# Performance work log

Hardware: AMD Instinct MI355X
Metric: run time of the kernel (lower is better)

## Reference

```python
import jax, jax.numpy as jnp
import numpy as np

N = 2000        # num_genes (nodes)
E = 64000       # edges
Q = 200000      # query edges
F_IN = 512      # num_features
H = 64          # hidden
Q_PHASE = 0.25  # magnetic charge q
SIM_DIM = 64
LABELS = 2


def _msconv(xr, xi, src, dst, w, W, n):
    """MagNet/MSGNN Chebyshev conv, K=1, sym normalization, absolute degree.

    A_s = (A + A^T)/2, Theta_ij = 2*pi*q*(A_ij - A_ji),
    L_hat = L - I = -D^{-1/2} A_s D^{-1/2} * exp(i*Theta)  (lambda_max = 2)
    out = X @ W[0] + (L_hat X) @ W[1]   (real weights on complex signal)
    """
    # symmetrize: each directed edge contributes entries (src->dst) and (dst->src)
    ss = jnp.concatenate([src, dst])
    dd = jnp.concatenate([dst, src])
    ws = jnp.concatenate([w, w]) * 0.5
    theta = 2.0 * jnp.pi * Q_PHASE * jnp.concatenate([w, -w])
    # absolute degree of symmetrized adjacency
    deg = jax.ops.segment_sum(jnp.abs(ws), dd, num_segments=n)
    dinv = jnp.where(deg > 0, 1.0 / jnp.sqrt(deg), 0.0)
    norm = ws * dinv[ss] * dinv[dd]
    cr = -norm * jnp.cos(theta)  # real part of L_hat entries
    ci = -norm * jnp.sin(theta)  # imag part
    xrs, xis = xr[ss], xi[ss]
    t1r = jax.ops.segment_sum(cr[:, None] * xrs - ci[:, None] * xis, dd, num_segments=n)
    t1i = jax.ops.segment_sum(cr[:, None] * xis + ci[:, None] * xrs, dd, num_segments=n)
    return xr @ W[0] + t1r @ W[1], xi @ W[0] + t1i @ W[1]


def setup_inputs() -> dict:
    key = jax.random.key(0)
    ks = jax.random.split(key, 10)
    real = jax.random.normal(ks[0], (N, F_IN), jnp.float32)
    imag = jax.random.normal(ks[1], (N, F_IN), jnp.float32)
    edge_index = jax.random.randint(ks[2], (2, E), 0, N, dtype=jnp.int64)
    query_edges = jax.random.randint(ks[3], (Q, 2), 0, N, dtype=jnp.int64)
    all_embeddings = jax.random.normal(ks[4], (N * N, SIM_DIM), jnp.float32)
    edge_weight = jax.random.uniform(ks[5], (E,), jnp.float32)
    W1 = jax.random.normal(ks[6], (2, F_IN, H), jnp.float32) / np.sqrt(F_IN)
    W2 = jax.random.normal(ks[7], (2, H, H), jnp.float32) / np.sqrt(H)
    lin_w = jax.random.normal(ks[8], (4 * H + SIM_DIM, LABELS), jnp.float32) * 0.05
    lin_b = jnp.zeros((LABELS,), jnp.float32)
    return {"real": real, "imag": imag, "edge_index": edge_index,
            "query_edges": query_edges, "all_embeddings": all_embeddings,
            "edge_weight": edge_weight, "W1": W1, "W2": W2,
            "lin_w": lin_w, "lin_b": lin_b}


def reference(real, imag, edge_index, query_edges, all_embeddings, edge_weight,
              W1, W2, lin_w, lin_b):
    src, dst = edge_index[0], edge_index[1]
    for W in (W1, W2):
        real, imag = _msconv(real, imag, src, dst, edge_weight, W, N)
        mask = (real >= 0).astype(real.dtype)   # complex_relu
        real = real * mask
        imag = imag * mask
    ni, nj = query_edges[:, 0], query_edges[:, 1]
    sim = all_embeddings[ni * N + nj]           # vectorized per-edge lookup
    x = jnp.concatenate([real[ni], real[nj], imag[ni], imag[nj], sim], axis=-1)
    # eval mode: dropout is identity
    logits = x @ lin_w + lin_b
    return jax.nn.log_softmax(logits, axis=1)
```

## Files before the change

kernel.cpp:

```cpp
#include <hip/hip_runtime.h>
#include <math.h>

constexpr int N_NODES = 2000;
constexpr int F_IN    = 512;
constexpr int H       = 64;
constexpr int SLOT_SH = 8;
constexpr int GBLK    = 1664;

__device__ __forceinline__ void gemm_tile256(
    const float* __restrict__ A, const float* __restrict__ W,
    float (*As)[33], float (*Ws)[64],
    int r0, int K, float* __restrict__ C)
{
  int t  = threadIdx.x;
  int tx = t & 15, ty = t >> 4;
  float acc[4][4] = {};
  for (int k0 = 0; k0 < K; k0 += 32) {
    #pragma unroll
    for (int i = 0; i < 8; i++) {
      int idx = t + i * 256;
      int row = idx >> 5, kk = idx & 31;
      int gr = r0 + row;
      As[row][kk] = (gr < N_NODES) ? A[(size_t)gr * K + k0 + kk] : 0.f;
    }
    #pragma unroll
    for (int i = 0; i < 8; i++) {
      int idx = t + i * 256;
      int kk = idx >> 6, col = idx & 63;
      Ws[kk][col] = W[(size_t)(k0 + kk) * H + col];
    }
    __syncthreads();
    #pragma unroll
    for (int kk = 0; kk < 32; kk++) {
      float4 wv = *reinterpret_cast<const float4*>(&Ws[kk][tx * 4]);
      float av[4];
      #pragma unroll
      for (int r = 0; r < 4; r++) av[r] = As[ty * 4 + r][kk];
      #pragma unroll
      for (int r = 0; r < 4; r++) {
        acc[r][0] = fmaf(av[r], wv.x, acc[r][0]);
        acc[r][1] = fmaf(av[r], wv.y, acc[r][1]);
        acc[r][2] = fmaf(av[r], wv.z, acc[r][2]);
        acc[r][3] = fmaf(av[r], wv.w, acc[r][3]);
      }
    }
    __syncthreads();
  }
  #pragma unroll
  for (int r = 0; r < 4; r++) {
    int gr = r0 + ty * 4 + r;
    if (gr < N_NODES) {
      *reinterpret_cast<float4*>(&C[(size_t)gr * H + tx * 4]) =
          make_float4(acc[r][0], acc[r][1], acc[r][2], acc[r][3]);
    }
  }
}

__global__ __launch_bounds__(256) void mega_kernel(
    const float* __restrict__ real, const float* __restrict__ imag,
    const float* __restrict__ W1,
    const int* __restrict__ ei, const float* __restrict__ ew,
    const int* __restrict__ qe, const float* __restrict__ emb,
    const float* __restrict__ lw,
    float* __restrict__ deg, int* __restrict__ cnt,
    int* __restrict__ nbr, float* __restrict__ cra, float* __restrict__ cia,
    float* __restrict__ P0r, float* __restrict__ P0i,
    float* __restrict__ P1r, float* __restrict__ P1i,
    float2* __restrict__ sl, int E, int Qn, int eblocks)
{
  __shared__ float As[64][33];
  __shared__ float Ws[32][64];
  int b = blockIdx.x;
  if (b < GBLK) {
    const float2* lw2 = reinterpret_cast<const float2*>(lw);
    int l = threadIdx.x & 15;
    float2 wa = lw2[256 + 4 * l];
    float2 wb = lw2[257 + 4 * l];
    float2 wc = lw2[258 + 4 * l];
    float2 wd = lw2[259 + 4 * l];
    int g0 = (b * 256 + threadIdx.x) >> 4;
    int ng = (GBLK * 256) >> 4;
    const float4* emb4 = reinterpret_cast<const float4*>(emb);
    for (int q = g0; q < Qn; q += 2 * ng) {
      int q2 = q + ng;
      bool has2 = q2 < Qn;
      int ni0 = qe[2 * q], nj0 = qe[2 * q + 1];
      int ni1 = has2 ? qe[2 * q2] : ni0;
      int nj1 = has2 ? qe[2 * q2 + 1] : nj0;
      float4 sa = emb4[((size_t)ni0 * N_NODES + nj0) * 16 + l];
      float4 sb = emb4[((size_t)ni1 * N_NODES + nj1) * 16 + l];
      float a0 = sa.x * wa.x + sa.y * wb.x + sa.z * wc.x + sa.w * wd.x;
      float a1 = sa.x * wa.y + sa.y * wb.y + sa.z * wc.y + sa.w * wd.y;
      float b0 = sb.x * wa.x + sb.y * wb.x + sb.z * wc.x + sb.w * wd.x;
      float b1 = sb.x * wa.y + sb.y * wb.y + sb.z * wc.y + sb.w * wd.y;
      #pragma unroll
      for (int off = 1; off < 16; off <<= 1) {
        a0 += __shfl_xor(a0, off, 64);
        a1 += __shfl_xor(a1, off, 64);
        b0 += __shfl_xor(b0, off, 64);
        b1 += __shfl_xor(b1, off, 64);
      }
      if (l == 0) {
        sl[q] = make_float2(a0, a1);
        if (has2) sl[q2] = make_float2(b0, b1);
      }
    }
  } else if (b < GBLK + eblocks) {
    int e = (b - GBLK) * 256 + threadIdx.x;
    if (e < E) {
      int s = ei[e], d = ei[E + e];
      float ww = ew[e];
      float aw = fabsf(0.5f * ww);
      atomicAdd(&deg[d], aw);
      atomicAdd(&deg[s], aw);
      float sn, cs;
      sincosf(1.5707963267948966f * ww, &sn, &cs);
      float cr = -0.5f * ww * cs;
      float ci = -0.5f * ww * sn;
      int p1 = atomicAdd(&cnt[d], 1);
      int i1 = (d << SLOT_SH) + p1;
      nbr[i1] = s; cra[i1] = cr; cia[i1] = ci;
      int p2 = atomicAdd(&cnt[s], 1);
      int i2 = (s << SLOT_SH) + p2;
      nbr[i2] = d; cra[i2] = cr; cia[i2] = -ci;
    }
  } else {
    int bi = b - GBLK - eblocks;
    int which = bi & 3, tile = bi >> 2;
    const float* A = (which & 1) ? imag : real;
    const float* W = W1 + (size_t)(which >> 1) * F_IN * H;
    float* C = (which == 0) ? P0r : (which == 1) ? P0i
             : (which == 2) ? P1r : P1i;
    gemm_tile256(A, W, As, Ws, tile * 64, F_IN, C);
  }
}

__device__ __forceinline__ void agg_partial(
    const int* __restrict__ cnt, const int* __restrict__ nbr,
    const float* __restrict__ cra, const float* __restrict__ cia,
    const float* __restrict__ deg,
    const float* __restrict__ Pr, const float* __restrict__ Pi,
    int v, int h, int wv, float& aro, float& aio)
{
  int cv = cnt[v];
  float ar = 0.f, ai = 0.f;
  for (int j = wv; j < cv; j += 4) {
    int idx = (v << SLOT_SH) + j;
    int u = nbr[idx];
    float dg = deg[u];
    float du = (dg > 0.f) ? rsqrtf(dg) : 0.f;
    float cr = cra[idx] * du, ci = cia[idx] * du;
    float pr = Pr[u * H + h];
    float pi = Pi[u * H + h];
    ar = fmaf(cr, pr, ar); ar = fmaf(-ci, pi, ar);
    ai = fmaf(cr, pi, ai); ai = fmaf( ci, pr, ai);
  }
  aro = ar; aio = ai;
}

__global__ __launch_bounds__(256) void aggregate1_kernel(
    const int* __restrict__ cnt, const int* __restrict__ nbr,
    const float* __restrict__ cra, const float* __restrict__ cia,
    const float* __restrict__ deg,
    const float* __restrict__ P0r, const float* __restrict__ P0i,
    const float* __restrict__ P1r, const float* __restrict__ P1i,
    float* __restrict__ xr, float* __restrict__ xi)
{
  __shared__ float sr[4][64], si[4][64];
  int v = blockIdx.x;
  int h = threadIdx.x & 63;
  int wv = threadIdx.x >> 6;
  float ar, ai;
  agg_partial(cnt, nbr, cra, cia, deg, P1r, P1i, v, h, wv, ar, ai);
  sr[wv][h] = ar; si[wv][h] = ai;
  __syncthreads();
  if (wv == 0) {
    float dgv = deg[v];
    float dv = (dgv > 0.f) ? rsqrtf(dgv) : 0.f;
    ar = (sr[0][h] + sr[1][h] + sr[2][h] + sr[3][h]) * dv + P0r[v * H + h];
    ai = (si[0][h] + si[1][h] + si[2][h] + si[3][h]) * dv + P0i[v * H + h];
    if (ar < 0.f) { ar = 0.f; ai = 0.f; }
    xr[v * H + h] = ar;
    xi[v * H + h] = ai;
  }
}

__global__ __launch_bounds__(256) void gemm2_kernel(
    const float* __restrict__ xr, const float* __restrict__ xi,
    const float* __restrict__ W2,
    float* __restrict__ P0r, float* __restrict__ P0i,
    float* __restrict__ P1r, float* __restrict__ P1i)
{
  __shared__ float As[64][33];
  __shared__ float Ws[32][64];
  int bi = blockIdx.x;
  int which = bi & 3, tile = bi >> 2;
  const float* A = (which & 1) ? xi : xr;
  const float* W = W2 + (size_t)(which >> 1) * H * H;
  float* C = (which == 0) ? P0r : (which == 1) ? P0i
           : (which == 2) ? P1r : P1i;
  gemm_tile256(A, W, As, Ws, tile * 64, H, C);
}

__global__ __launch_bounds__(256) void aggregate2_kernel(
    const int* __restrict__ cnt, const int* __restrict__ nbr,
    const float* __restrict__ cra, const float* __restrict__ cia,
    const float* __restrict__ deg,
    const float* __restrict__ P0r, const float* __restrict__ P0i,
    const float* __restrict__ P1r, const float* __restrict__ P1i,
    const float* __restrict__ lw, const float* __restrict__ lb,
    float4* __restrict__ nuw)
{
  __shared__ float sr[4][64], si[4][64];
  int v = blockIdx.x;
  int h = threadIdx.x & 63;
  int wv = threadIdx.x >> 6;
  float ar, ai;
  agg_partial(cnt, nbr, cra, cia, deg, P1r, P1i, v, h, wv, ar, ai);
  sr[wv][h] = ar; si[wv][h] = ai;
  __syncthreads();
  if (wv == 0) {
    float dgv = deg[v];
    float dv = (dgv > 0.f) ? rsqrtf(dgv) : 0.f;
    ar = (sr[0][h] + sr[1][h] + sr[2][h] + sr[3][h]) * dv + P0r[v * H + h];
    ai = (si[0][h] + si[1][h] + si[2][h] + si[3][h]) * dv + P0i[v * H + h];
    if (ar < 0.f) { ar = 0.f; ai = 0.f; }
    const float2* lw2 = reinterpret_cast<const float2*>(lw);
    float2 l0 = lw2[h], l1 = lw2[64 + h], l2 = lw2[128 + h], l3 = lw2[192 + h];
    float u0 = ar * l0.x + ai * l2.x;
    float u1 = ar * l0.y + ai * l2.y;
    float w0 = ar * l1.x + ai * l3.x;
    float w1 = ar * l1.y + ai * l3.y;
    #pragma unroll
    for (int off = 1; off < 64; off <<= 1) {
      u0 += __shfl_xor(u0, off, 64);
      u1 += __shfl_xor(u1, off, 64);
      w0 += __shfl_xor(w0, off, 64);
      w1 += __shfl_xor(w1, off, 64);
    }
    if (h == 0)
      nuw[v] = make_float4(u0 + lb[0], u1 + lb[1], w0, w1);
  }
}

__global__ __launch_bounds__(256) void head_kernel(
    const int* __restrict__ qe, const float2* __restrict__ sl,
    const float4* __restrict__ nuw, float2* __restrict__ out, int Qn)
{
  int q = blockIdx.x * 256 + threadIdx.x;
  if (q >= Qn) return;
  int2 nij = reinterpret_cast<const int2*>(qe)[q];
  float2 s = sl[q];
  float4 ui = nuw[nij.x];
  float4 wj = nuw[nij.y];
  float lg0 = s.x + ui.x + wj.z;
  float lg1 = s.y + ui.y + wj.w;
  float m = fmaxf(lg0, lg1);
  float lse = m + logf(expf(lg0 - m) + expf(lg1 - m));
  out[q] = make_float2(lg0 - lse, lg1 - lse);
}

extern "C" void kernel_launch(void* const* d_in, const int* in_sizes, int n_in,
                              void* d_out, int out_size, void* d_ws, size_t ws_size,
                              hipStream_t stream)
{
  const float* real = (const float*)d_in[0];
  const float* imag = (const float*)d_in[1];
  const int*   ei   = (const int*)d_in[2];
  const int*   qe   = (const int*)d_in[3];
  const float* emb  = (const float*)d_in[4];
  const float* ew   = (const float*)d_in[5];
  const float* W1   = (const float*)d_in[6];
  const float* W2   = (const float*)d_in[7];
  const float* lw   = (const float*)d_in[8];
  const float* lb   = (const float*)d_in[9];
  float2* out = (float2*)d_out;

  int E = in_sizes[2] / 2;
  int Q = in_sizes[3] / 2;
  int n = N_NODES;
  int nslots = N_NODES << SLOT_SH;

  char* ws = (char*)d_ws;
  size_t off = 0;
  auto alloc = [&](size_t bytes) -> char* {
    char* p = ws + off;
    off = (off + bytes + 255) & ~(size_t)255;
    return p;
  };
  float*  deg = (float*)alloc(2048 * 4);
  int*    cnt = (int*)  alloc(2048 * 4);
  int*    nbr = (int*)  alloc((size_t)nslots * 4);
  float*  cra = (float*)alloc((size_t)nslots * 4);
  float*  cia = (float*)alloc((size_t)nslots * 4);
  float*  P0r = (float*)alloc((size_t)n * H * 4);
  float*  P0i = (float*)alloc((size_t)n * H * 4);
  float*  P1r = (float*)alloc((size_t)n * H * 4);
  float*  P1i = (float*)alloc((size_t)n * H * 4);
  float*  xr1 = (float*)alloc((size_t)n * H * 4);
  float*  xi1 = (float*)alloc((size_t)n * H * 4);
  float4* nuw = (float4*)alloc((size_t)n * 16);
  float2* sl  = (float2*)alloc((size_t)Q * 8);

  hipMemsetAsync(deg, 0, 2 * 2048 * 4, stream);

  int eblocks = (E + 255) / 256;
  mega_kernel<<<GBLK + eblocks + 128, 256, 0, stream>>>(
      real, imag, W1, ei, ew, qe, emb, lw,
      deg, cnt, nbr, cra, cia, P0r, P0i, P1r, P1i, sl, E, Q, eblocks);
  aggregate1_kernel<<<n, 256, 0, stream>>>(cnt, nbr, cra, cia, deg,
                                           P0r, P0i, P1r, P1i, xr1, xi1);
  gemm2_kernel<<<128, 256, 0, stream>>>(xr1, xi1, W2, P0r, P0i, P1r, P1i);
  aggregate2_kernel<<<n, 256, 0, stream>>>(cnt, nbr, cra, cia, deg,
                                           P0r, P0i, P1r, P1i, lw, lb, nuw);
  head_kernel<<<(Q + 255) / 256, 256, 0, stream>>>(qe, sl, nuw, out, Q);
}
```

Before: 145.2 us.

## Sort queries by source node before gathering embedding rows

Removes the embedding gather from the fused first kernel. Queries are now counting-sorted by source node with a histogram, a scan and a scatter pass, and a separate gather kernel reads embedding rows in sorted order, 8 queries per group. Rows sharing the same ni then lie within one 2000-row region of the 1 GB table, which should improve DRAM page/TLB locality and allow more loads in flight. The cost is three extra kernels, atomics, and losing the overlap of the gather with the graph work.

```diff
diff --git a/kernel.cpp b/kernel.cpp
--- a/kernel.cpp
+++ b/kernel.cpp
@@ -5,7 +5,7 @@
 constexpr int F_IN    = 512;
 constexpr int H       = 64;
 constexpr int SLOT_SH = 8;
-constexpr int GBLK    = 1664;
+constexpr int QHB     = 200;
 
 __device__ __forceinline__ void gemm_tile256(
     const float* __restrict__ A, const float* __restrict__ W,
@@ -60,53 +60,18 @@
     const float* __restrict__ real, const float* __restrict__ imag,
     const float* __restrict__ W1,
     const int* __restrict__ ei, const float* __restrict__ ew,
-    const int* __restrict__ qe, const float* __restrict__ emb,
-    const float* __restrict__ lw,
-    float* __restrict__ deg, int* __restrict__ cnt,
+    const int* __restrict__ qe,
+    float* __restrict__ deg, int* __restrict__ cnt, int* __restrict__ qcnt,
     int* __restrict__ nbr, float* __restrict__ cra, float* __restrict__ cia,
     float* __restrict__ P0r, float* __restrict__ P0i,
     float* __restrict__ P1r, float* __restrict__ P1i,
-    float2* __restrict__ sl, int E, int Qn, int eblocks)
+    int E, int Qn, int eblocks)
 {
   __shared__ float As[64][33];
   __shared__ float Ws[32][64];
   int b = blockIdx.x;
-  if (b < GBLK) {
-    const float2* lw2 = reinterpret_cast<const float2*>(lw);
-    int l = threadIdx.x & 15;
-    float2 wa = lw2[256 + 4 * l];
-    float2 wb = lw2[257 + 4 * l];
-    float2 wc = lw2[258 + 4 * l];
-    float2 wd = lw2[259 + 4 * l];
-    int g0 = (b * 256 + threadIdx.x) >> 4;
-    int ng = (GBLK * 256) >> 4;
-    const float4* emb4 = reinterpret_cast<const float4*>(emb);
-    for (int q = g0; q < Qn; q += 2 * ng) {
-      int q2 = q + ng;
-      bool has2 = q2 < Qn;
-      int ni0 = qe[2 * q], nj0 = qe[2 * q + 1];
-      int ni1 = has2 ? qe[2 * q2] : ni0;
-      int nj1 = has2 ? qe[2 * q2 + 1] : nj0;
-      float4 sa = emb4[((size_t)ni0 * N_NODES + nj0) * 16 + l];
-      float4 sb = emb4[((size_t)ni1 * N_NODES + nj1) * 16 + l];
-      float a0 = sa.x * wa.x + sa.y * wb.x + sa.z * wc.x + sa.w * wd.x;
-      float a1 = sa.x * wa.y + sa.y * wb.y + sa.z * wc.y + sa.w * wd.y;
-      float b0 = sb.x * wa.x + sb.y * wb.x + sb.z * wc.x + sb.w * wd.x;
-      float b1 = sb.x * wa.y + sb.y * wb.y + sb.z * wc.y + sb.w * wd.y;
-      #pragma unroll
-      for (int off = 1; off < 16; off <<= 1) {
-        a0 += __shfl_xor(a0, off, 64);
-        a1 += __shfl_xor(a1, off, 64);
-        b0 += __shfl_xor(b0, off, 64);
-        b1 += __shfl_xor(b1, off, 64);
-      }
-      if (l == 0) {
-        sl[q] = make_float2(a0, a1);
-        if (has2) sl[q2] = make_float2(b0, b1);
-      }
-    }
-  } else if (b < GBLK + eblocks) {
-    int e = (b - GBLK) * 256 + threadIdx.x;
+  if (b < eblocks) {
+    int e = b * 256 + threadIdx.x;
     if (e < E) {
       int s = ei[e], d = ei[E + e];
       float ww = ew[e];
@@ -124,15 +89,56 @@
       int i2 = (s << SLOT_SH) + p2;
       nbr[i2] = d; cra[i2] = cr; cia[i2] = -ci;
     }
-  } else {
-    int bi = b - GBLK - eblocks;
+  } else if (b < eblocks + 128) {
+    int bi = b - eblocks;
     int which = bi & 3, tile = bi >> 2;
     const float* A = (which & 1) ? imag : real;
     const float* W = W1 + (size_t)(which >> 1) * F_IN * H;
     float* C = (which == 0) ? P0r : (which == 1) ? P0i
              : (which == 2) ? P1r : P1i;
     gemm_tile256(A, W, As, Ws, tile * 64, F_IN, C);
-  }
+  } else {
+    int b2 = b - eblocks - 128;
+    for (int q = b2 * 256 + threadIdx.x; q < Qn; q += QHB * 256)
+      atomicAdd(&qcnt[qe[2 * q]], 1);
+  }
+}
+
+__global__ __launch_bounds__(1024) void scan_kernel(
+    const int* __restrict__ cnt, int* __restrict__ fillpos, int n)
+{
+  __shared__ int bufA[2048], bufB[2048];
+  int t = threadIdx.x;
+  bufA[t]        = (t < n) ? cnt[t] : 0;
+  bufA[t + 1024] = (t + 1024 < n) ? cnt[t + 1024] : 0;
+  __syncthreads();
+  int* src = bufA; int* dst = bufB;
+  for (int d = 1; d < 2048; d <<= 1) {
+    #pragma unroll
+    for (int k = 0; k < 2; k++) {
+      int i = t + k * 1024;
+      int v = src[i];
+      if (i >= d) v += src[i - d];
+      dst[i] = v;
+    }
+    __syncthreads();
+    int* tmp = src; src = dst; dst = tmp;
+  }
+  for (int k = 0; k < 2; k++) {
+    int i = t + k * 1024;
+    if (i < n) fillpos[i] = (i == 0) ? 0 : src[i - 1];
+  }
+}
+
+__global__ __launch_bounds__(256) void scatter_kernel(
+    const int* __restrict__ qe, int* __restrict__ qfill,
+    int* __restrict__ perm, int Qn)
+{
+  int q = blockIdx.x * 256 + threadIdx.x;
+  if (q >= Qn) return;
+  int ni = qe[2 * q];
+  int pos = atomicAdd(&qfill[ni], 1);
+  perm[pos] = q;
 }
 
 __device__ __forceinline__ void agg_partial(
@@ -243,6 +249,51 @@
   }
 }
 
+__global__ __launch_bounds__(256) void gather_kernel(
+    const int* __restrict__ perm, const int* __restrict__ qe,
+    const float* __restrict__ emb, const float* __restrict__ lw,
+    float2* __restrict__ sl, int Qn)
+{
+  const float2* lw2 = reinterpret_cast<const float2*>(lw);
+  int l = threadIdx.x & 15;
+  float2 wa = lw2[256 + 4 * l];
+  float2 wb = lw2[257 + 4 * l];
+  float2 wc = lw2[258 + 4 * l];
+  float2 wd = lw2[259 + 4 * l];
+  int grp  = (blockIdx.x * 256 + threadIdx.x) >> 4;
+  int ngrp = (gridDim.x * 256) >> 4;
+  const float4* emb4 = reinterpret_cast<const float4*>(emb);
+  const int2* qe2 = reinterpret_cast<const int2*>(qe);
+  for (int p0 = grp * 8; p0 < Qn; p0 += ngrp * 8) {
+    int nq = (Qn - p0 >= 8) ? 8 : (Qn - p0);
+    int sq[8];
+    float4 s[8];
+    #pragma unroll
+    for (int k = 0; k < 8; k++)
+      if (k < nq) sq[k] = perm[p0 + k];
+    #pragma unroll
+    for (int k = 0; k < 8; k++) {
+      if (k < nq) {
+        int2 nij = qe2[sq[k]];
+        s[k] = emb4[((size_t)nij.x * N_NODES + nij.y) * 16 + l];
+      }
+    }
+    #pragma unroll
+    for (int k = 0; k < 8; k++) {
+      if (k < nq) {
+        float a0 = s[k].x * wa.x + s[k].y * wb.x + s[k].z * wc.x + s[k].w * wd.x;
+        float a1 = s[k].x * wa.y + s[k].y * wb.y + s[k].z * wc.y + s[k].w * wd.y;
+        #pragma unroll
+        for (int off = 1; off < 16; off <<= 1) {
+          a0 += __shfl_xor(a0, off, 64);
+          a1 += __shfl_xor(a1, off, 64);
+        }
+        if (l == 0) sl[sq[k]] = make_float2(a0, a1);
+      }
+    }
+  }
+}
+
 __global__ __launch_bounds__(256) void head_kernel(
     const int* __restrict__ qe, const float2* __restrict__ sl,
     const float4* __restrict__ nuw, float2* __restrict__ out, int Qn)
@@ -288,30 +339,36 @@
     off = (off + bytes + 255) & ~(size_t)255;
     return p;
   };
-  float*  deg = (float*)alloc(2048 * 4);
-  int*    cnt = (int*)  alloc(2048 * 4);
-  int*    nbr = (int*)  alloc((size_t)nslots * 4);
-  float*  cra = (float*)alloc((size_t)nslots * 4);
-  float*  cia = (float*)alloc((size_t)nslots * 4);
-  float*  P0r = (float*)alloc((size_t)n * H * 4);
-  float*  P0i = (float*)alloc((size_t)n * H * 4);
-  float*  P1r = (float*)alloc((size_t)n * H * 4);
-  float*  P1i = (float*)alloc((size_t)n * H * 4);
-  float*  xr1 = (float*)alloc((size_t)n * H * 4);
-  float*  xi1 = (float*)alloc((size_t)n * H * 4);
-  float4* nuw = (float4*)alloc((size_t)n * 16);
-  float2* sl  = (float2*)alloc((size_t)Q * 8);
-
-  hipMemsetAsync(deg, 0, 2 * 2048 * 4, stream);
+  float*  deg  = (float*)alloc(2048 * 4);
+  int*    cnt  = (int*)  alloc(2048 * 4);
+  int*    qcnt = (int*)  alloc(2048 * 4);
+  int*    qfil = (int*)  alloc(2048 * 4);
+  int*    nbr  = (int*)  alloc((size_t)nslots * 4);
+  float*  cra  = (float*)alloc((size_t)nslots * 4);
+  float*  cia  = (float*)alloc((size_t)nslots * 4);
+  float*  P0r  = (float*)alloc((size_t)n * H * 4);
+  float*  P0i  = (float*)alloc((size_t)n * H * 4);
+  float*  P1r  = (float*)alloc((size_t)n * H * 4);
+  float*  P1i  = (float*)alloc((size_t)n * H * 4);
+  float*  xr1  = (float*)alloc((size_t)n * H * 4);
+  float*  xi1  = (float*)alloc((size_t)n * H * 4);
+  float4* nuw  = (float4*)alloc((size_t)n * 16);
+  int*    perm = (int*)  alloc((size_t)Q * 4);
+  float2* sl   = (float2*)alloc((size_t)Q * 8);
+
+  hipMemsetAsync(deg, 0, 3 * 2048 * 4, stream);
 
   int eblocks = (E + 255) / 256;
-  mega_kernel<<<GBLK + eblocks + 128, 256, 0, stream>>>(
-      real, imag, W1, ei, ew, qe, emb, lw,
-      deg, cnt, nbr, cra, cia, P0r, P0i, P1r, P1i, sl, E, Q, eblocks);
+  mega_kernel<<<eblocks + 128 + QHB, 256, 0, stream>>>(
+      real, imag, W1, ei, ew, qe,
+      deg, cnt, qcnt, nbr, cra, cia, P0r, P0i, P1r, P1i, E, Q, eblocks);
+  scan_kernel<<<1, 1024, 0, stream>>>(qcnt, qfil, n);
+  scatter_kernel<<<(Q + 255) / 256, 256, 0, stream>>>(qe, qfil, perm, Q);
   aggregate1_kernel<<<n, 256, 0, stream>>>(cnt, nbr, cra, cia, deg,
                                            P0r, P0i, P1r, P1i, xr1, xi1);
   gemm2_kernel<<<128, 256, 0, stream>>>(xr1, xi1, W2, P0r, P0i, P1r, P1i);
   aggregate2_kernel<<<n, 256, 0, stream>>>(cnt, nbr, cra, cia, deg,
                                            P0r, P0i, P1r, P1i, lw, lb, nuw);
+  gather_kernel<<<1563, 256, 0, stream>>>(perm, qe, emb, lw, sl, Q);
   head_kernel<<<(Q + 255) / 256, 256, 0, stream>>>(qe, sl, nuw, out, Q);
 }
```

Result: slower. 194.4 us (+33.9%).

## Move embedding gather from mega kernel into fused gather-head kernel

Applied to the files above, without the earlier changes.

Removes the similarity-embedding gather from the first fused kernel and performs it at the end in a new kernel that also computes the final logits and log-softmax, eliminating the intermediate sl buffer and the separate head launch. Each 16-lane group now issues eight independent embedding row loads before reducing, to increase memory-level parallelism. The edge preprocessing also switches to the fast __sincosf intrinsic. The trade-off is that the large random gather no longer overlaps with the GEMM and edge-processing phase and instead runs serially after aggregation.

```diff
diff --git a/kernel.cpp b/kernel.cpp
--- a/kernel.cpp
+++ b/kernel.cpp
@@ -5,7 +5,6 @@
 constexpr int F_IN    = 512;
 constexpr int H       = 64;
 constexpr int SLOT_SH = 8;
-constexpr int GBLK    = 1664;
 
 __device__ __forceinline__ void gemm_tile256(
     const float* __restrict__ A, const float* __restrict__ W,
@@ -60,53 +59,16 @@
     const float* __restrict__ real, const float* __restrict__ imag,
     const float* __restrict__ W1,
     const int* __restrict__ ei, const float* __restrict__ ew,
-    const int* __restrict__ qe, const float* __restrict__ emb,
-    const float* __restrict__ lw,
     float* __restrict__ deg, int* __restrict__ cnt,
     int* __restrict__ nbr, float* __restrict__ cra, float* __restrict__ cia,
     float* __restrict__ P0r, float* __restrict__ P0i,
-    float* __restrict__ P1r, float* __restrict__ P1i,
-    float2* __restrict__ sl, int E, int Qn, int eblocks)
+    float* __restrict__ P1r, float* __restrict__ P1i, int E, int eblocks)
 {
   __shared__ float As[64][33];
   __shared__ float Ws[32][64];
   int b = blockIdx.x;
-  if (b < GBLK) {
-    const float2* lw2 = reinterpret_cast<const float2*>(lw);
-    int l = threadIdx.x & 15;
-    float2 wa = lw2[256 + 4 * l];
-    float2 wb = lw2[257 + 4 * l];
-    float2 wc = lw2[258 + 4 * l];
-    float2 wd = lw2[259 + 4 * l];
-    int g0 = (b * 256 + threadIdx.x) >> 4;
-    int ng = (GBLK * 256) >> 4;
-    const float4* emb4 = reinterpret_cast<const float4*>(emb);
-    for (int q = g0; q < Qn; q += 2 * ng) {
-      int q2 = q + ng;
-      bool has2 = q2 < Qn;
-      int ni0 = qe[2 * q], nj0 = qe[2 * q + 1];
-      int ni1 = has2 ? qe[2 * q2] : ni0;
-      int nj1 = has2 ? qe[2 * q2 + 1] : nj0;
-      float4 sa = emb4[((size_t)ni0 * N_NODES + nj0) * 16 + l];
-      float4 sb = emb4[((size_t)ni1 * N_NODES + nj1) * 16 + l];
-      float a0 = sa.x * wa.x + sa.y * wb.x + sa.z * wc.x + sa.w * wd.x;
-      float a1 = sa.x * wa.y + sa.y * wb.y + sa.z * wc.y + sa.w * wd.y;
-      float b0 = sb.x * wa.x + sb.y * wb.x + sb.z * wc.x + sb.w * wd.x;
-      float b1 = sb.x * wa.y + sb.y * wb.y + sb.z * wc.y + sb.w * wd.y;
-      #pragma unroll
-      for (int off = 1; off < 16; off <<= 1) {
-        a0 += __shfl_xor(a0, off, 64);
-        a1 += __shfl_xor(a1, off, 64);
-        b0 += __shfl_xor(b0, off, 64);
-        b1 += __shfl_xor(b1, off, 64);
-      }
-      if (l == 0) {
-        sl[q] = make_float2(a0, a1);
-        if (has2) sl[q2] = make_float2(b0, b1);
-      }
-    }
-  } else if (b < GBLK + eblocks) {
-    int e = (b - GBLK) * 256 + threadIdx.x;
+  if (b < eblocks) {
+    int e = b * 256 + threadIdx.x;
     if (e < E) {
       int s = ei[e], d = ei[E + e];
       float ww = ew[e];
@@ -114,7 +76,7 @@
       atomicAdd(&deg[d], aw);
       atomicAdd(&deg[s], aw);
       float sn, cs;
-      sincosf(1.5707963267948966f * ww, &sn, &cs);
+      __sincosf(1.5707963267948966f * ww, &sn, &cs);
       float cr = -0.5f * ww * cs;
       float ci = -0.5f * ww * sn;
       int p1 = atomicAdd(&cnt[d], 1);
@@ -125,7 +87,7 @@
       nbr[i2] = d; cra[i2] = cr; cia[i2] = -ci;
     }
   } else {
-    int bi = b - GBLK - eblocks;
+    int bi = b - eblocks;
     int which = bi & 3, tile = bi >> 2;
     const float* A = (which & 1) ? imag : real;
     const float* W = W1 + (size_t)(which >> 1) * F_IN * H;
@@ -243,21 +205,56 @@
   }
 }
 
-__global__ __launch_bounds__(256) void head_kernel(
-    const int* __restrict__ qe, const float2* __restrict__ sl,
-    const float4* __restrict__ nuw, float2* __restrict__ out, int Qn)
-{
-  int q = blockIdx.x * 256 + threadIdx.x;
-  if (q >= Qn) return;
-  int2 nij = reinterpret_cast<const int2*>(qe)[q];
-  float2 s = sl[q];
-  float4 ui = nuw[nij.x];
-  float4 wj = nuw[nij.y];
-  float lg0 = s.x + ui.x + wj.z;
-  float lg1 = s.y + ui.y + wj.w;
-  float m = fmaxf(lg0, lg1);
-  float lse = m + logf(expf(lg0 - m) + expf(lg1 - m));
-  out[q] = make_float2(lg0 - lse, lg1 - lse);
+__global__ __launch_bounds__(256) void gather_head_kernel(
+    const int* __restrict__ qe, const float* __restrict__ emb,
+    const float* __restrict__ lw, const float4* __restrict__ nuw,
+    const float* __restrict__ lb, float2* __restrict__ out, int Qn)
+{
+  const float2* lw2 = reinterpret_cast<const float2*>(lw);
+  int l = threadIdx.x & 15;
+  float2 wa = lw2[256 + 4 * l];
+  float2 wb = lw2[257 + 4 * l];
+  float2 wc = lw2[258 + 4 * l];
+  float2 wd = lw2[259 + 4 * l];
+  int grp  = (blockIdx.x * 256 + threadIdx.x) >> 4;
+  int ngrp = (gridDim.x * 256) >> 4;
+  const float4* emb4 = reinterpret_cast<const float4*>(emb);
+  const int2*   qe2  = reinterpret_cast<const int2*>(qe);
+  for (int p0 = grp * 8; p0 < Qn; p0 += ngrp * 8) {
+    int nq = (Qn - p0 >= 8) ? 8 : (Qn - p0);
+    float4 s[8];
+    #pragma unroll
+    for (int k = 0; k < 8; k++) {
+      if (k < nq) {
+        int2 nij = qe2[p0 + k];
+        s[k] = emb4[((size_t)nij.x * N_NODES + nij.y) * 16 + l];
+      }
+    }
+    float r0 = 0.f, r1 = 0.f;
+    #pragma unroll
+    for (int k = 0; k < 8; k++) {
+      if (k < nq) {
+        float a0 = s[k].x * wa.x + s[k].y * wb.x + s[k].z * wc.x + s[k].w * wd.x;
+        float a1 = s[k].x * wa.y + s[k].y * wb.y + s[k].z * wc.y + s[k].w * wd.y;
+        #pragma unroll
+        for (int off = 1; off < 16; off <<= 1) {
+          a0 += __shfl_xor(a0, off, 64);
+          a1 += __shfl_xor(a1, off, 64);
+        }
+        if (l == k) { r0 = a0; r1 = a1; }
+      }
+    }
+    if (l < nq) {
+      int2 nij = qe2[p0 + l];
+      float4 ui = nuw[nij.x];
+      float4 wj = nuw[nij.y];
+      float lg0 = r0 + ui.x + wj.z;
+      float lg1 = r1 + ui.y + wj.w;
+      float m = fmaxf(lg0, lg1);
+      float lse = m + logf(expf(lg0 - m) + expf(lg1 - m));
+      out[p0 + l] = make_float2(lg0 - lse, lg1 - lse);
+    }
+  }
 }
 
 extern "C" void kernel_launch(void* const* d_in, const int* in_sizes, int n_in,
@@ -300,18 +297,17 @@
   float*  xr1 = (float*)alloc((size_t)n * H * 4);
   float*  xi1 = (float*)alloc((size_t)n * H * 4);
   float4* nuw = (float4*)alloc((size_t)n * 16);
-  float2* sl  = (float2*)alloc((size_t)Q * 8);
 
   hipMemsetAsync(deg, 0, 2 * 2048 * 4, stream);
 
   int eblocks = (E + 255) / 256;
-  mega_kernel<<<GBLK + eblocks + 128, 256, 0, stream>>>(
-      real, imag, W1, ei, ew, qe, emb, lw,
-      deg, cnt, nbr, cra, cia, P0r, P0i, P1r, P1i, sl, E, Q, eblocks);
+  mega_kernel<<<eblocks + 128, 256, 0, stream>>>(
+      real, imag, W1, ei, ew, deg, cnt, nbr, cra, cia,
+      P0r, P0i, P1r, P1i, E, eblocks);
   aggregate1_kernel<<<n, 256, 0, stream>>>(cnt, nbr, cra, cia, deg,
                                            P0r, P0i, P1r, P1i, xr1, xi1);
   gemm2_kernel<<<128, 256, 0, stream>>>(xr1, xi1, W2, P0r, P0i, P1r, P1i);
   aggregate2_kernel<<<n, 256, 0, stream>>>(cnt, nbr, cra, cia, deg,
                                            P0r, P0i, P1r, P1i, lw, lb, nuw);
-  head_kernel<<<(Q + 255) / 256, 256, 0, stream>>>(qe, sl, nuw, out, Q);
-}
+  gather_head_kernel<<<1563, 256, 0, stream>>>(qe, emb, lw, nuw, lb, out, Q);
+}
```

New measurement: 149.9 us. +3.3%, slower.
